# Optimization experiments

Measured on AMD Instinct MI355X. Metric: run time of the kernel, lower is better.

## Reference

```python
import jax, jax.numpy as jnp
import numpy as np

B, S, D, L = 2, 1024, 1024, 48
K = max(1, int(L * 0.1))  # = 4, matches torch k = max(1, int(num_paths * 0.1))
EPS = 1e-5  # torch LayerNorm default


def setup_inputs() -> dict:
    key = jax.random.key(0)
    ks = jax.random.split(key, 7)
    inv = 1.0 / np.sqrt(D).astype(np.float32)
    return {
        "x": jax.random.normal(ks[0], (B, S, D), jnp.float32),
        "gate_w": jax.random.normal(ks[1], (L, D), jnp.float32) * inv,          # gate_proj weight [L,D], no bias
        "lattice_weights": jax.random.normal(ks[2], (L, D, D), jnp.float32) * 0.02,
        "out_w": jax.random.normal(ks[3], (D, D), jnp.float32) * inv,            # out_proj weight [D,D]
        "out_b": jnp.zeros((D,), jnp.float32),
        "ln_g": jnp.ones((D,), jnp.float32),
        "ln_b": jnp.zeros((D,), jnp.float32),
    }


def reference(x, gate_w, lattice_weights, out_w, out_b, ln_g, ln_b):
    # Gate: top-k routing over L lattice paths
    logits = jnp.einsum('bsd,ld->bsl', x, gate_w)                 # [B,S,L]
    top_vals, idx = jax.lax.top_k(logits, K)                      # [B,S,K] each (descending, like torch.topk)
    scores = jax.nn.softmax(top_vals, axis=-1)                    # [B,S,K]

    # Mathematically identical to gathering [B,S,K,D,D] expert matrices and
    # weight-summing, but computed as one dense GEMM over all L experts
    # followed by a cheap gather -- avoids the 32GB intermediate.
    out_all = jnp.einsum('bsd,lde->bsle', x, lattice_weights)     # [B,S,L,D]
    sel = jnp.take_along_axis(out_all, idx[..., None], axis=2)    # [B,S,K,D]
    lattice_out = jnp.einsum('bskd,bsk->bsd', sel, scores)        # [B,S,D]

    y = x + jnp.einsum('bsd,ed->bse', lattice_out, out_w) + out_b # residual + out_proj
    mu = jnp.mean(y, axis=-1, keepdims=True)
    var = jnp.mean((y - mu) ** 2, axis=-1, keepdims=True)
    return ln_g * (y - mu) * jax.lax.rsqrt(var + EPS) + ln_b
```

## Files before the change

### kernel.cpp

```cpp
#include <hip/hip_runtime.h>
#include <stdint.h>

#define TT 2048
#define DD 1024
#define LL 48

typedef __attribute__((ext_vector_type(8))) short short8;
typedef __attribute__((ext_vector_type(4))) float f32x4;

static __device__ __forceinline__ unsigned int f2bf(float f) {
  union { float f; unsigned int u; } v; v.f = f;
  return (v.u + 0x7FFFu + ((v.u >> 16) & 1u)) >> 16;
}
static __device__ __forceinline__ unsigned int pack2(float a, float b) {
  return f2bf(a) | (f2bf(b) << 16);
}

typedef __attribute__((address_space(1))) const void* as1_t;
typedef __attribute__((address_space(3))) void* as3_t;
static __device__ __forceinline__ void gll16(const void* g, void* s) {
  __builtin_amdgcn_global_load_lds((as1_t)g, (as3_t)s, 16, 0, 0);
}

__global__ __launch_bounds__(256) void k_gate(
    const float* __restrict__ x, const float* __restrict__ gw,
    unsigned short* __restrict__ xb,
    int* __restrict__ counts, int* __restrict__ btok, float* __restrict__ bscore)
{
  __shared__ float xs[8][1024];
  __shared__ float lg[8][48];
  const int tid = threadIdx.x;
  const int t0 = blockIdx.x * 8;
  for (int u = tid; u < 2048; u += 256) {
    int tok = u >> 8;
    int c = (u & 255) << 2;
    float4 v = *(const float4*)(x + (size_t)(t0 + tok) * DD + c);
    *(float4*)&xs[tok][c] = v;
    uint2 p; p.x = pack2(v.x, v.y); p.y = pack2(v.z, v.w);
    *(uint2*)(xb + (size_t)(t0 + tok) * DD + c) = p;
  }
  __syncthreads();
  const int lane = tid & 63, wid = tid >> 6;
  for (int li = 0; li < 12; ++li) {
    const int l = wid + (li << 2);
    const float4* gp = (const float4*)(gw + (size_t)l * DD);
    float4 g0 = gp[lane], g1 = gp[lane + 64], g2 = gp[lane + 128], g3 = gp[lane + 192];
    for (int tok = 0; tok < 8; ++tok) {
      const float4* xp = (const float4*)&xs[tok][0];
      float4 a0 = xp[lane], a1 = xp[lane + 64], a2 = xp[lane + 128], a3 = xp[lane + 192];
      float s = a0.x*g0.x + a0.y*g0.y + a0.z*g0.z + a0.w*g0.w
              + a1.x*g1.x + a1.y*g1.y + a1.z*g1.z + a1.w*g1.w
              + a2.x*g2.x + a2.y*g2.y + a2.z*g2.z + a2.w*g2.w
              + a3.x*g3.x + a3.y*g3.y + a3.z*g3.z + a3.w*g3.w;
      #pragma unroll
      for (int off = 32; off; off >>= 1) s += __shfl_down(s, off);
      if (lane == 0) lg[tok][l] = s;
    }
  }
  __syncthreads();
  if (tid < 8) {
    const int tok = tid;
    float v[4]; int id[4];
    unsigned long long taken = 0ull;
    for (int k = 0; k < 4; ++k) {
      float best = -3.4e38f; int bi = 0;
      for (int l = 0; l < 48; ++l) {
        float cand = lg[tok][l];
        if (!((taken >> l) & 1ull) && cand > best) { best = cand; bi = l; }
      }
      taken |= (1ull << bi); v[k] = best; id[k] = bi;
    }
    float e1 = expf(v[1] - v[0]);
    float e2 = expf(v[2] - v[0]);
    float e3 = expf(v[3] - v[0]);
    float inv = 1.0f / (1.0f + e1 + e2 + e3);
    float sc[4] = { inv, e1*inv, e2*inv, e3*inv };
    for (int k = 0; k < 4; ++k) {
      int pos = atomicAdd(&counts[id[k]], 1);
      btok[id[k] * TT + pos] = ((t0 + tok) << 2) | k;
      bscore[id[k] * TT + pos] = sc[k];
    }
  }
}

__global__ __launch_bounds__(512, 4) void k_expert(
    const unsigned short* __restrict__ xb, const float* __restrict__ W,
    const int* __restrict__ counts, const int* __restrict__ btok,
    const float* __restrict__ bscore, float* __restrict__ sel)
{
  const int l = blockIdx.z;
  const int ncnt = counts[l];
  const int m0 = blockIdx.y * 256;
  if (m0 >= ncnt) return;
  const int n0 = blockIdx.x * 128;
  const int tid = threadIdx.x, lane = tid & 63, wid = tid >> 6;
  const int wr = wid & 3, wc = wid >> 2;

  __shared__ alignas(16) unsigned short As[2][256 * 32];
  __shared__ alignas(16) float           Bs[2][32 * 128];
  __shared__ int   toks[256];
  __shared__ float scs[256];

  if (tid < 256) {
    int r = m0 + tid;
    toks[tid] = (r < ncnt) ? btok[l * TT + r] : 0;
    scs[tid]  = (r < ncnt) ? bscore[l * TT + r] : 0.f;
  }
  __syncthreads();

  const unsigned short* asrc0 = xb + (size_t)(toks[tid >> 2]       >> 2) * DD + (tid & 3) * 8;
  const unsigned short* asrc1 = xb + (size_t)(toks[128 + (tid >> 2)] >> 2) * DD + (tid & 3) * 8;
  const float* Wl = W + (size_t)l * DD * DD + n0;
  const int d0 = tid >> 5, cu = tid & 31;
  const int d1 = d0 + 16;
  const float* bsrc0 = Wl + (size_t)d0 * DD + ((cu ^ (((d0 >> 3) & 1) << 2)) << 2);
  const float* bsrc1 = Wl + (size_t)d1 * DD + ((cu ^ (((d1 >> 3) & 1) << 2)) << 2);

  f32x4 acc[4][4];
  #pragma unroll
  for (int m = 0; m < 4; ++m)
    #pragma unroll
    for (int n = 0; n < 4; ++n)
      #pragma unroll
      for (int j = 0; j < 4; ++j) acc[m][n][j] = 0.f;

#define STAGE(buf, k0) do { \
    gll16(asrc0 + (k0), &As[buf][tid * 8]); \
    gll16(asrc1 + (k0), &As[buf][(512 + tid) * 8]); \
    gll16(bsrc0 + (size_t)(k0) * DD, &Bs[buf][tid * 4]); \
    gll16(bsrc1 + (size_t)(k0) * DD, &Bs[buf][(512 + tid) * 4]); \
  } while (0)

  const int fr = lane & 15, fq = lane >> 4;
  const int bkey = (fq & 1) << 4;

  STAGE(0, 0);
  __syncthreads();
  int cur = 0;
  for (int t = 0; t < 32; ++t) {
    if (t < 31) STAGE(cur ^ 1, (t + 1) * 32);
    const unsigned short* Ab = As[cur];
    const float* Bb = Bs[cur];
    short8 af[4], bf[4];
    #pragma unroll
    for (int m = 0; m < 4; ++m)
      af[m] = *(const short8*)(Ab + (wr * 64 + m * 16 + fr) * 32 + fq * 8);
    #pragma unroll
    for (int n = 0; n < 4; ++n) {
      const float* bp = Bb + (size_t)fq * 8 * 128 + ((wc * 64 + n * 16 + fr) ^ bkey);
      float w0 = bp[0],       w1 = bp[128],     w2 = bp[256],     w3 = bp[384];
      float w4 = bp[512],     w5 = bp[640],     w6 = bp[768],     w7 = bp[896];
      uint4 pv;
      pv.x = pack2(w0, w1); pv.y = pack2(w2, w3);
      pv.z = pack2(w4, w5); pv.w = pack2(w6, w7);
      bf[n] = *(short8*)&pv;
    }
    #pragma unroll
    for (int m = 0; m < 4; ++m)
      #pragma unroll
      for (int n = 0; n < 4; ++n)
        acc[m][n] = __builtin_amdgcn_mfma_f32_16x16x32_bf16(af[m], bf[n], acc[m][n], 0, 0, 0);
    __syncthreads();
    cur ^= 1;
  }
#undef STAGE

  #pragma unroll
  for (int m = 0; m < 4; ++m) {
    #pragma unroll
    for (int j = 0; j < 4; ++j) {
      const int r = wr * 64 + m * 16 + fq * 4 + j;
      if (m0 + r < ncnt) {
        const float sc = scs[r];
        const size_t ob = (size_t)toks[r] * DD + n0 + wc * 64 + fr;
        #pragma unroll
        for (int n = 0; n < 4; ++n)
          sel[ob + n * 16] = acc[m][n][j] * sc;
      }
    }
  }
}

__global__ __launch_bounds__(256) void k_combine(const float* __restrict__ sel,
                                                 unsigned short* __restrict__ lat)
{
  const size_t i = ((size_t)blockIdx.x * 256 + threadIdx.x) << 2;
  const size_t t = i >> 10, d = i & 1023;
  const float* p = sel + ((t << 2) << 10) + d;
  float4 s0 = *(const float4*)(p);
  float4 s1 = *(const float4*)(p + 1024);
  float4 s2 = *(const float4*)(p + 2048);
  float4 s3 = *(const float4*)(p + 3072);
  float r0 = s0.x + s1.x + s2.x + s3.x;
  float r1 = s0.y + s1.y + s2.y + s3.y;
  float r2 = s0.z + s1.z + s2.z + s3.z;
  float r3 = s0.w + s1.w + s2.w + s3.w;
  uint2 pk; pk.x = pack2(r0, r1); pk.y = pack2(r2, r3);
  *(uint2*)(lat + i) = pk;
}

__global__ __launch_bounds__(256, 2) void k_outproj(
    const unsigned short* __restrict__ lat, const float* __restrict__ W2,
    const float* __restrict__ xres, const float* __restrict__ bias,
    float* __restrict__ y)
{
  const int n0 = blockIdx.x * 64;
  const int m0 = blockIdx.y * 128;
  const int tid = threadIdx.x, lane = tid & 63, wid = tid >> 6;

  __shared__ alignas(16) unsigned short As[2][128][40];
  __shared__ alignas(16) unsigned short Bs[2][64][40];

  const int aq = tid >> 2, aseg = tid & 3;
  const unsigned short* la0 = lat + (size_t)(m0 + aq) * DD + aseg * 8;
  const unsigned short* la1 = lat + (size_t)(m0 + aq + 64) * DD + aseg * 8;
  const int be = tid >> 2, bks = tid & 3;
  const float* wb = W2 + (size_t)(n0 + be) * DD + bks * 8;

  f32x4 acc[2][4];
  #pragma unroll
  for (int m = 0; m < 2; ++m)
    #pragma unroll
    for (int n = 0; n < 4; ++n)
      #pragma unroll
      for (int j = 0; j < 4; ++j) acc[m][n][j] = 0.f;

  int4 av0, av1;
  float4 w0, w1;

#define O_LOAD(kk) do { \
    av0 = *(const int4*)(la0 + (kk)); \
    av1 = *(const int4*)(la1 + (kk)); \
    w0 = *(const float4*)(wb + (kk)); \
    w1 = *(const float4*)(wb + (kk) + 4); \
  } while (0)

#define O_STORE(b) do { \
    *(int4*)&As[b][aq][aseg * 8]      = av0; \
    *(int4*)&As[b][aq + 64][aseg * 8] = av1; \
    uint4 pv; \
    pv.x = pack2(w0.x, w0.y); pv.y = pack2(w0.z, w0.w); \
    pv.z = pack2(w1.x, w1.y); pv.w = pack2(w1.z, w1.w); \
    *(uint4*)&Bs[b][be][bks * 8] = pv; \
  } while (0)

  O_LOAD(0); O_STORE(0); __syncthreads();
  int cur = 0;
  for (int t = 0; t < 32; ++t) {
    const bool more = (t < 31);
    if (more) O_LOAD((t + 1) * 32);
    short8 af[2], bf[4];
    #pragma unroll
    for (int n = 0; n < 4; ++n)
      bf[n] = *(const short8*)&Bs[cur][n * 16 + (lane & 15)][(lane >> 4) * 8];
    #pragma unroll
    for (int m = 0; m < 2; ++m)
      af[m] = *(const short8*)&As[cur][wid * 32 + m * 16 + (lane & 15)][(lane >> 4) * 8];
    #pragma unroll
    for (int m = 0; m < 2; ++m)
      #pragma unroll
      for (int n = 0; n < 4; ++n)
        acc[m][n] = __builtin_amdgcn_mfma_f32_16x16x32_bf16(af[m], bf[n], acc[m][n], 0, 0, 0);
    if (more) O_STORE(cur ^ 1);
    __syncthreads();
    cur ^= 1;
  }
#undef O_LOAD
#undef O_STORE

  #pragma unroll
  for (int m = 0; m < 2; ++m) {
    #pragma unroll
    for (int j = 0; j < 4; ++j) {
      const int t = m0 + wid * 32 + m * 16 + ((lane >> 4) << 2) + j;
      #pragma unroll
      for (int n = 0; n < 4; ++n) {
        const int e = n0 + n * 16 + (lane & 15);
        y[(size_t)t * DD + e] = xres[(size_t)t * DD + e] + acc[m][n][j] + bias[e];
      }
    }
  }
}

__global__ __launch_bounds__(256) void k_ln(const float* __restrict__ y,
    const float* __restrict__ g, const float* __restrict__ b, float* __restrict__ out)
{
  const int t = blockIdx.x, tid = threadIdx.x;
  float4 v = *(const float4*)(y + (size_t)t * DD + tid * 4);
  float s  = v.x + v.y + v.z + v.w;
  float ss = v.x*v.x + v.y*v.y + v.z*v.z + v.w*v.w;
  #pragma unroll
  for (int off = 32; off; off >>= 1) { s += __shfl_down(s, off); ss += __shfl_down(ss, off); }
  __shared__ float rs[8];
  const int wid = tid >> 6, lane = tid & 63;
  if (lane == 0) { rs[wid] = s; rs[wid + 4] = ss; }
  __syncthreads();
  float S  = rs[0] + rs[1] + rs[2] + rs[3];
  float SS = rs[4] + rs[5] + rs[6] + rs[7];
  float mu = S * (1.0f / DD);
  float var = SS * (1.0f / DD) - mu * mu;
  float inv = rsqrtf(var + 1e-5f);
  float4 gg = *(const float4*)(g + tid * 4);
  float4 bb = *(const float4*)(b + tid * 4);
  float4 o;
  o.x = gg.x * (v.x - mu) * inv + bb.x;
  o.y = gg.y * (v.y - mu) * inv + bb.y;
  o.z = gg.z * (v.z - mu) * inv + bb.z;
  o.w = gg.w * (v.w - mu) * inv + bb.w;
  *(float4*)(out + (size_t)t * DD + tid * 4) = o;
}

extern "C" void kernel_launch(void* const* d_in, const int* in_sizes, int n_in,
                              void* d_out, int out_size, void* d_ws, size_t ws_size,
                              hipStream_t stream) {
  (void)in_sizes; (void)n_in; (void)out_size;
  const float* x   = (const float*)d_in[0];
  const float* gw  = (const float*)d_in[1];
  const float* lw  = (const float*)d_in[2];
  const float* ow  = (const float*)d_in[3];
  const float* obv = (const float*)d_in[4];
  const float* lng = (const float*)d_in[5];
  const float* lnb = (const float*)d_in[6];
  float* out = (float*)d_out;
  char* ws = (char*)d_ws;

  unsigned short* xb     = (unsigned short*)(ws);
  unsigned short* lat    = (unsigned short*)(ws + (4ull << 20));
  float*          y      = (float*)(ws + (8ull << 20));
  float*          sel    = (float*)(ws + (16ull << 20));
  int*            counts = (int*)(ws + (48ull << 20));
  int*            btok   = (int*)(ws + (48ull << 20) + 4096);
  float*          bscore = (float*)(ws + (48ull << 20) + 4096 + (size_t)LL * TT * 4);
  if (ws_size < ((48ull << 20) + 4096 + 2ull * LL * TT * 4)) return;

  hipMemsetAsync(counts, 0, LL * sizeof(int), stream);
  k_gate<<<TT / 8, 256, 0, stream>>>(x, gw, xb, counts, btok, bscore);
  k_expert<<<dim3(8, 2, LL), 512, 0, stream>>>(xb, lw, counts, btok, bscore, sel);
  k_combine<<<TT * DD / (256 * 4), 256, 0, stream>>>(sel, lat);
  k_outproj<<<dim3(16, 16), 256, 0, stream>>>(lat, ow, x, obv, y);
  k_ln<<<TT, 256, 0, stream>>>(y, lng, lnb, out);
}
```

Before: 212.7 us.

## Convert expert weights to bf16 once at stage time with padded LDS layout

The expert GEMM now uses a 256x64 tile with 256 threads, which doubles the grid along N. Expert weights are loaded into registers and converted to packed bf16 pairs before being written to a padded (stride 17) shared-memory layout. Previously fp32 weights were async-copied into LDS and every wave re-converted them on each k-step. Each wave now reads B fragments as single short8 loads, cutting LDS traffic and repeated conversion work. In exchange the weight prefetch goes through registers instead of the direct-to-LDS path, which may lengthen the exposed latency. The A tile (256 rows) is also reloaded for twice as many N-blocks.

```diff
diff --git a/kernel.cpp b/kernel.cpp
--- a/kernel.cpp
+++ b/kernel.cpp
@@ -83,7 +83,7 @@
   }
 }
 
-__global__ __launch_bounds__(512, 4) void k_expert(
+__global__ __launch_bounds__(256, 3) void k_expert(
     const unsigned short* __restrict__ xb, const float* __restrict__ W,
     const int* __restrict__ counts, const int* __restrict__ btok,
     const float* __restrict__ bscore, float* __restrict__ sel)
@@ -92,29 +92,30 @@
   const int ncnt = counts[l];
   const int m0 = blockIdx.y * 256;
   if (m0 >= ncnt) return;
-  const int n0 = blockIdx.x * 128;
-  const int tid = threadIdx.x, lane = tid & 63, wid = tid >> 6;
-  const int wr = wid & 3, wc = wid >> 2;
+  const int n0 = blockIdx.x * 64;
+  const int tid = threadIdx.x, lane = tid & 63, wr = tid >> 6;
 
   __shared__ alignas(16) unsigned short As[2][256 * 32];
-  __shared__ alignas(16) float           Bs[2][32 * 128];
+  __shared__ alignas(16) unsigned int   Bs[2][64 * 17];
   __shared__ int   toks[256];
   __shared__ float scs[256];
 
-  if (tid < 256) {
+  {
     int r = m0 + tid;
     toks[tid] = (r < ncnt) ? btok[l * TT + r] : 0;
     scs[tid]  = (r < ncnt) ? bscore[l * TT + r] : 0.f;
   }
   __syncthreads();
 
-  const unsigned short* asrc0 = xb + (size_t)(toks[tid >> 2]       >> 2) * DD + (tid & 3) * 8;
-  const unsigned short* asrc1 = xb + (size_t)(toks[128 + (tid >> 2)] >> 2) * DD + (tid & 3) * 8;
-  const float* Wl = W + (size_t)l * DD * DD + n0;
-  const int d0 = tid >> 5, cu = tid & 31;
-  const int d1 = d0 + 16;
-  const float* bsrc0 = Wl + (size_t)d0 * DD + ((cu ^ (((d0 >> 3) & 1) << 2)) << 2);
-  const float* bsrc1 = Wl + (size_t)d1 * DD + ((cu ^ (((d1 >> 3) & 1) << 2)) << 2);
+  const unsigned short* asrc[4];
+  #pragma unroll
+  for (int i = 0; i < 4; ++i) {
+    int u = i * 256 + tid;
+    asrc[i] = xb + (size_t)(toks[u >> 2] >> 2) * DD + (u & 3) * 8;
+  }
+  const int bp = tid >> 4, be0 = (tid & 15) * 4;
+  const float* wsrc0 = W + (size_t)l * DD * DD + (size_t)(2 * bp) * DD + n0 + be0;
+  const float* wsrc1 = wsrc0 + DD;
 
   f32x4 acc[4][4];
   #pragma unroll
@@ -124,46 +125,54 @@
       #pragma unroll
       for (int j = 0; j < 4; ++j) acc[m][n][j] = 0.f;
 
-#define STAGE(buf, k0) do { \
-    gll16(asrc0 + (k0), &As[buf][tid * 8]); \
-    gll16(asrc1 + (k0), &As[buf][(512 + tid) * 8]); \
-    gll16(bsrc0 + (size_t)(k0) * DD, &Bs[buf][tid * 4]); \
-    gll16(bsrc1 + (size_t)(k0) * DD, &Bs[buf][(512 + tid) * 4]); \
+  float4 bw0, bw1;
+
+#define BLOAD(k0) do { \
+    bw0 = *(const float4*)(wsrc0 + (size_t)(k0) * DD); \
+    bw1 = *(const float4*)(wsrc1 + (size_t)(k0) * DD); \
+  } while (0)
+
+#define ASTAGE(buf, k0) do { \
+    _Pragma("unroll") \
+    for (int i = 0; i < 4; ++i) \
+      gll16(asrc[i] + (k0), &As[buf][(i * 256 + tid) * 8]); \
+  } while (0)
+
+#define BSTORE(buf) do { \
+    Bs[buf][(be0 + 0) * 17 + bp] = pack2(bw0.x, bw1.x); \
+    Bs[buf][(be0 + 1) * 17 + bp] = pack2(bw0.y, bw1.y); \
+    Bs[buf][(be0 + 2) * 17 + bp] = pack2(bw0.z, bw1.z); \
+    Bs[buf][(be0 + 3) * 17 + bp] = pack2(bw0.w, bw1.w); \
   } while (0)
 
   const int fr = lane & 15, fq = lane >> 4;
-  const int bkey = (fq & 1) << 4;
-
-  STAGE(0, 0);
+
+  BLOAD(0); ASTAGE(0, 0); BSTORE(0);
   __syncthreads();
   int cur = 0;
   for (int t = 0; t < 32; ++t) {
-    if (t < 31) STAGE(cur ^ 1, (t + 1) * 32);
+    if (t < 31) { BLOAD((t + 1) * 32); ASTAGE(cur ^ 1, (t + 1) * 32); }
     const unsigned short* Ab = As[cur];
-    const float* Bb = Bs[cur];
+    const unsigned short* Bb = (const unsigned short*)Bs[cur];
     short8 af[4], bf[4];
     #pragma unroll
     for (int m = 0; m < 4; ++m)
       af[m] = *(const short8*)(Ab + (wr * 64 + m * 16 + fr) * 32 + fq * 8);
     #pragma unroll
-    for (int n = 0; n < 4; ++n) {
-      const float* bp = Bb + (size_t)fq * 8 * 128 + ((wc * 64 + n * 16 + fr) ^ bkey);
-      float w0 = bp[0],       w1 = bp[128],     w2 = bp[256],     w3 = bp[384];
-      float w4 = bp[512],     w5 = bp[640],     w6 = bp[768],     w7 = bp[896];
-      uint4 pv;
-      pv.x = pack2(w0, w1); pv.y = pack2(w2, w3);
-      pv.z = pack2(w4, w5); pv.w = pack2(w6, w7);
-      bf[n] = *(short8*)&pv;
-    }
+    for (int n = 0; n < 4; ++n)
+      bf[n] = *(const short8*)(Bb + ((n * 16 + fr) * 17 + fq * 4) * 2);
     #pragma unroll
     for (int m = 0; m < 4; ++m)
       #pragma unroll
       for (int n = 0; n < 4; ++n)
         acc[m][n] = __builtin_amdgcn_mfma_f32_16x16x32_bf16(af[m], bf[n], acc[m][n], 0, 0, 0);
+    if (t < 31) BSTORE(cur ^ 1);
     __syncthreads();
     cur ^= 1;
   }
-#undef STAGE
+#undef BLOAD
+#undef ASTAGE
+#undef BSTORE
 
   #pragma unroll
   for (int m = 0; m < 4; ++m) {
@@ -172,7 +181,7 @@
       const int r = wr * 64 + m * 16 + fq * 4 + j;
       if (m0 + r < ncnt) {
         const float sc = scs[r];
-        const size_t ob = (size_t)toks[r] * DD + n0 + wc * 64 + fr;
+        const size_t ob = (size_t)toks[r] * DD + n0 + fr;
         #pragma unroll
         for (int n = 0; n < 4; ++n)
           sel[ob + n * 16] = acc[m][n][j] * sc;
@@ -335,7 +344,7 @@
 
   hipMemsetAsync(counts, 0, LL * sizeof(int), stream);
   k_gate<<<TT / 8, 256, 0, stream>>>(x, gw, xb, counts, btok, bscore);
-  k_expert<<<dim3(8, 2, LL), 512, 0, stream>>>(xb, lw, counts, btok, bscore, sel);
+  k_expert<<<dim3(16, 2, LL), 256, 0, stream>>>(xb, lw, counts, btok, bscore, sel);
   k_combine<<<TT * DD / (256 * 4), 256, 0, stream>>>(sel, lat);
   k_outproj<<<dim3(16, 16), 256, 0, stream>>>(lat, ow, x, obv, y);
   k_ln<<<TT, 256, 0, stream>>>(y, lng, lnb, out);
```

Result: slower. 242.2 us (+13.9%).
